# Optimization experiments

Measured on AMD Instinct MI355X. Metric: run time of the kernel, lower is better.

## Reference

```python
import jax, jax.numpy as jnp
import numpy as np

NH = 8        # num_heads
KS = 64       # key_size
C_IN = 256
C_OUT = 3 * NH * KS   # 1536
GROUPS = 3 * NH       # 24
EPS = 1e-5
H = W = 64


def setup_inputs() -> dict:
    key = jax.random.key(0)
    k1, k2 = jax.random.split(key)
    x = jax.random.normal(k1, (1, C_IN, H, W), dtype=jnp.float32)
    conv_w = jax.random.normal(k2, (C_OUT, C_IN, 1, 1), dtype=jnp.float32) * 0.05
    gn_w = jnp.ones((C_OUT,), dtype=jnp.float32)
    gn_b = jnp.zeros((C_OUT,), dtype=jnp.float32)
    return {"x": x, "conv_w": conv_w, "gn_w": gn_w, "gn_b": gn_b}


def reference(x, conv_w, gn_w, gn_b):
    B, _, h, w = x.shape
    # 1x1 conv (normalize=True -> no bias): per-pixel GEMM over channels
    attn = jnp.einsum('bchw,oc->bohw', x, conv_w[:, :, 0, 0])  # [B, 1536, H, W]
    # GroupNorm: 24 groups of KS channels, normalized over (KS, H, W)
    g = attn.reshape(B, GROUPS, -1)
    mean = g.mean(axis=-1, keepdims=True)
    var = g.var(axis=-1, keepdims=True)
    g = (g - mean) * jax.lax.rsqrt(var + EPS)
    attn = g.reshape(B, C_OUT, h, w) * gn_w[None, :, None, None] + gn_b[None, :, None, None]
    # split into key, query, value (in that order, per chunk(3, dim=2))
    attn = attn.reshape(B, NH, 3 * KS, h * w)
    key_, query, value = jnp.split(attn, 3, axis=2)   # each [B, NH, KS, HW]
    # saliency = q^T @ k / sqrt(KS) -> [B, NH, HW, HW]
    saliency = jnp.einsum('bnkq,bnkl->bnql', query, key_) / jnp.sqrt(jnp.float32(KS))
    mask = jax.nn.softmax(saliency, axis=-1)
    # out = v @ mask^T -> [B, NH, KS, HW]
    out = jnp.einsum('bnkl,bnql->bnkq', value, mask)
    return out.reshape(B, NH * KS, h, w)
```

## Files before the change

kernel.cpp:

```cpp
#include <hip/hip_runtime.h>

typedef __bf16 bf16;
typedef __bf16 bf16x8 __attribute__((ext_vector_type(8)));
typedef __bf16 bf16x4 __attribute__((ext_vector_type(4)));
typedef float f32x4 __attribute__((ext_vector_type(4)));
typedef float f32x16 __attribute__((ext_vector_type(16)));


#define QF 0.18033688011112042f
#define EXPF(x) __builtin_amdgcn_exp2f(x)
#define MFMA32(A, B, C) __builtin_amdgcn_mfma_f32_32x32x16_bf16(A, B, C, 0, 0, 0)

union U4 { bf16x4 v; unsigned u[2]; };
union U8 { bf16x8 v; unsigned u[4]; };

__global__ void k_misc(const float* __restrict__ x, const float* __restrict__ w,
                       bf16* __restrict__ xT, bf16* __restrict__ wb, float* __restrict__ cs) {
    int b = blockIdx.x;
    if (b < 256) {
        __shared__ float ld[64][65];
        int cb = (b & 3) * 64;
        int pb = (b >> 2) * 64;
        int tp = (threadIdx.x & 15) * 4;
        int tc = threadIdx.x >> 4;
#pragma unroll
        for (int pass = 0; pass < 4; pass++) {
            int c = tc + pass * 16;
            float4 f = *(const float4*)(x + (cb + c) * 4096 + pb + tp);
            ld[tp][c] = f.x; ld[tp + 1][c] = f.y; ld[tp + 2][c] = f.z; ld[tp + 3][c] = f.w;
        }
        __syncthreads();
        int px = threadIdx.x >> 3;
        int co = (threadIdx.x & 7) * 8;
#pragma unroll
        for (int pass = 0; pass < 2; pass++) {
            int p2 = px + pass * 32;
            bf16x8 o;
#pragma unroll
            for (int j = 0; j < 8; j++) o[j] = (bf16)ld[p2][co + j];
            *(bf16x8*)(xT + (pb + p2) * 256 + cb + co) = o;
        }
    } else if (b < 640) {
        int idx = ((b - 256) * 256 + threadIdx.x) * 4;
        float4 f = *(const float4*)(w + idx);
        bf16x4 o;
        o[0] = (bf16)f.x; o[1] = (bf16)f.y; o[2] = (bf16)f.z; o[3] = (bf16)f.w;
        *(bf16x4*)(wb + idx) = o;
    } else {
#pragma unroll
        for (int i = 0; i < 12; i++) cs[i * 256 + threadIdx.x] = 0.f;
    }
}

__global__ __launch_bounds__(256) void k_conv(const bf16* __restrict__ Wb,
                                              const bf16* __restrict__ xT,
                                              bf16* __restrict__ qkvT,
                                              float* __restrict__ cs) {
    __shared__ __attribute__((aligned(16))) bf16 xs[64 * 72];
    __shared__ __attribute__((aligned(16))) bf16 ws2[64 * 72];
    int wid = threadIdx.x >> 6, lane = threadIdx.x & 63;
    int quad = lane >> 4, l15 = lane & 15;
    int g  = blockIdx.x % 24;
    int pb = (blockIdx.x / 24) * 64;
    int h = g / 3, sec = g % 3;
    int ob = g * 64;

    int srow = threadIdx.x >> 2;
    int scol = (threadIdx.x & 3) * 16;

    f32x4 acc[4];
#pragma unroll
    for (int c = 0; c < 4; c++) acc[c] = (f32x4){0.f, 0.f, 0.f, 0.f};

    bf16x8 fx0 = *(const bf16x8*)(xT + (pb + srow) * 256 + scol);
    bf16x8 fx1 = *(const bf16x8*)(xT + (pb + srow) * 256 + scol + 8);
    bf16x8 fw0 = *(const bf16x8*)(Wb + (ob + srow) * 256 + scol);
    bf16x8 fw1 = *(const bf16x8*)(Wb + (ob + srow) * 256 + scol + 8);

    for (int c4 = 0; c4 < 4; c4++) {
        __syncthreads();
        *(bf16x8*)(xs  + srow * 72 + scol)     = fx0;
        *(bf16x8*)(xs  + srow * 72 + scol + 8) = fx1;
        *(bf16x8*)(ws2 + srow * 72 + scol)     = fw0;
        *(bf16x8*)(ws2 + srow * 72 + scol + 8) = fw1;
        __syncthreads();

        if (c4 < 3) {
            int co = (c4 + 1) * 64;
            fx0 = *(const bf16x8*)(xT + (pb + srow) * 256 + co + scol);
            fx1 = *(const bf16x8*)(xT + (pb + srow) * 256 + co + scol + 8);
            fw0 = *(const bf16x8*)(Wb + (ob + srow) * 256 + co + scol);
            fw1 = *(const bf16x8*)(Wb + (ob + srow) * 256 + co + scol + 8);
        }

#pragma unroll
        for (int k2 = 0; k2 < 2; k2++) {
            bf16x8 a = *(const bf16x8*)(ws2 + (wid * 16 + l15) * 72 + k2 * 32 + quad * 8);
#pragma unroll
            for (int c = 0; c < 4; c++) {
                bf16x8 b = *(const bf16x8*)(xs + (c * 16 + l15) * 72 + k2 * 32 + quad * 8);
                acc[c] = __builtin_amdgcn_mfma_f32_16x16x32_bf16(a, b, acc[c], 0, 0, 0);
            }
        }
    }

    int ch0 = wid * 16 + quad * 4;
#pragma unroll
    for (int r = 0; r < 4; r++) {
        float sp  = acc[0][r] + acc[1][r] + acc[2][r] + acc[3][r];
        float ssp = acc[0][r] * acc[0][r] + acc[1][r] * acc[1][r]
                  + acc[2][r] * acc[2][r] + acc[3][r] * acc[3][r];
#pragma unroll
        for (int m = 1; m < 16; m <<= 1) {
            sp  += __shfl_xor(sp,  m, 64);
            ssp += __shfl_xor(ssp, m, 64);
        }
        if (l15 == 0) {
            atomicAdd(cs + (ob + ch0 + r) * 2,     sp);
            atomicAdd(cs + (ob + ch0 + r) * 2 + 1, ssp);
        }
    }

    __syncthreads();
    bf16* tile = xs;
    if (sec == 2) {
#pragma unroll
        for (int c = 0; c < 4; c++)
#pragma unroll
            for (int r = 0; r < 4; r++)
                tile[(ch0 + r) * 72 + c * 16 + l15] = (bf16)acc[c][r];
    } else {
#pragma unroll
        for (int c = 0; c < 4; c++) {
            bf16x4 o;
#pragma unroll
            for (int r = 0; r < 4; r++) o[r] = (bf16)acc[c][r];
            *(bf16x4*)(&tile[(c * 16 + l15) * 72 + ch0]) = o;
        }
    }
    __syncthreads();
    bf16* base = qkvT + h * 786432;
    int t = threadIdx.x;
    if (sec == 2) {
        bf16* V = base + 524288;
#pragma unroll
        for (int it = 0; it < 2; it++) {
            int e = it * 256 + t; int ch = e >> 3; int pxo = (e & 7) * 8;
            *(bf16x8*)(V + ch * 4096 + pb + pxo) = *(const bf16x8*)(&tile[ch * 72 + pxo]);
        }
    } else {
        bf16* dst = base + (sec == 0 ? 262144 : 0);
#pragma unroll
        for (int it = 0; it < 2; it++) {
            int e = it * 256 + t; int px = e >> 3; int cho = (e & 7) * 8;
            *(bf16x8*)(dst + (pb + px) * 64 + cho) = *(const bf16x8*)(&tile[px * 72 + cho]);
        }
    }
}

#define PF_BLOCK(S, LACC, PFA, PFB)                                             \
    {                                                                           \
        float p0 = EXPF(S[0]),  p1 = EXPF(S[1]),  p2 = EXPF(S[2]),  p3 = EXPF(S[3]);   \
        float p4 = EXPF(S[4]),  p5 = EXPF(S[5]),  p6 = EXPF(S[6]),  p7 = EXPF(S[7]);   \
        float p8 = EXPF(S[8]),  p9 = EXPF(S[9]),  p10 = EXPF(S[10]), p11 = EXPF(S[11]); \
        float p12 = EXPF(S[12]), p13 = EXPF(S[13]), p14 = EXPF(S[14]), p15 = EXPF(S[15]); \
        LACC += (((p0 + p1) + (p2 + p3)) + ((p4 + p5) + (p6 + p7)))             \
              + (((p8 + p9) + (p10 + p11)) + ((p12 + p13) + (p14 + p15)));      \
        U4 lo, hi;                                                              \
        lo.v[0] = (bf16)p0;  lo.v[1] = (bf16)p1;  lo.v[2] = (bf16)p2;  lo.v[3] = (bf16)p3;  \
        hi.v[0] = (bf16)p4;  hi.v[1] = (bf16)p5;  hi.v[2] = (bf16)p6;  hi.v[3] = (bf16)p7;  \
        unsigned a0 = lo.u[0], b0 = hi.u[0], a1 = lo.u[1], b1 = hi.u[1];        \
        asm("v_permlane32_swap_b32 %0, %1" : "+v"(a0), "+v"(b0));               \
        asm("v_permlane32_swap_b32 %0, %1" : "+v"(a1), "+v"(b1));               \
        U8 fA; fA.u[0] = a0; fA.u[1] = a1; fA.u[2] = b0; fA.u[3] = b1;          \
        PFA = fA.v;                                                             \
        U4 lo2, hi2;                                                            \
        lo2.v[0] = (bf16)p8;  lo2.v[1] = (bf16)p9;  lo2.v[2] = (bf16)p10; lo2.v[3] = (bf16)p11; \
        hi2.v[0] = (bf16)p12; hi2.v[1] = (bf16)p13; hi2.v[2] = (bf16)p14; hi2.v[3] = (bf16)p15; \
        unsigned a2 = lo2.u[0], b2 = hi2.u[0], a3 = lo2.u[1], b3 = hi2.u[1];    \
        asm("v_permlane32_swap_b32 %0, %1" : "+v"(a2), "+v"(b2));               \
        asm("v_permlane32_swap_b32 %0, %1" : "+v"(a3), "+v"(b3));               \
        U8 fB; fB.u[0] = a2; fB.u[1] = a3; fB.u[2] = b2; fB.u[3] = b3;          \
        PFB = fB.v;                                                             \
    }

#define STAGE(BK, BV)                                                           \
    *(bf16x8*)((BK) + r0 * 72 + koff)        = kf0;                             \
    *(bf16x8*)((BK) + (r0 + 32) * 72 + koff) = kf1;                             \
    *(bf16x8*)((BV) + r0 * 72 + koff)        = vf0;                             \
    *(bf16x8*)((BV) + (r0 + 32) * 72 + koff) = vf1;

#define PREFETCH(T)                                                             \
    {   int nb = (T) * 64;                                                      \
        kf0 = *(const bf16x8*)(KT + (nb + r0) * 64 + koff);                     \
        kf1 = *(const bf16x8*)(KT + (nb + r0 + 32) * 64 + koff);                \
        vf0 = *(const bf16x8*)(V + r0 * 4096 + nb + koff);                      \
        vf1 = *(const bf16x8*)(V + (r0 + 32) * 4096 + nb + koff); }

#define QK64(KSB)                                                               \
    {   const bf16* kra = (KSB) + l31 * 72 + half * 8;                          \
        const bf16* krb = (KSB) + (32 + l31) * 72 + half * 8;                   \
        __builtin_amdgcn_s_setprio(1);                                          \
        { bf16x8 fa = *(const bf16x8*)(kra +  0), fb = *(const bf16x8*)(krb +  0); \
          s00 = MFMA32(fa, bqA[0], s00); s01 = MFMA32(fa, bqB[0], s01);         \
          s10 = MFMA32(fb, bqA[0], s10); s11 = MFMA32(fb, bqB[0], s11); }       \
        { bf16x8 fa = *(const bf16x8*)(kra + 16), fb = *(const bf16x8*)(krb + 16); \
          s00 = MFMA32(fa, bqA[1], s00); s01 = MFMA32(fa, bqB[1], s01);         \
          s10 = MFMA32(fb, bqA[1], s10); s11 = MFMA32(fb, bqB[1], s11); }       \
        { bf16x8 fa = *(const bf16x8*)(kra + 32), fb = *(const bf16x8*)(krb + 32); \
          s00 = MFMA32(fa, bqA[2], s00); s01 = MFMA32(fa, bqB[2], s01);         \
          s10 = MFMA32(fb, bqA[2], s10); s11 = MFMA32(fb, bqB[2], s11); }       \
        { bf16x8 fa = *(const bf16x8*)(kra + 48), fb = *(const bf16x8*)(krb + 48); \
          s00 = MFMA32(fa, bqA[3], s00); s01 = MFMA32(fa, bqB[3], s01);         \
          s10 = MFMA32(fb, bqA[3], s10); s11 = MFMA32(fb, bqB[3], s11); }       \
        __builtin_amdgcn_s_setprio(0); }

#define PV64(VSB)                                                               \
    {   const bf16* vra = (VSB) + l31 * 72 + half * 8;                          \
        const bf16* vrb = (VSB) + (32 + l31) * 72 + half * 8;                   \
        __builtin_amdgcn_s_setprio(1);                                          \
        { bf16x8 fa = *(const bf16x8*)(vra +  0), fb = *(const bf16x8*)(vrb +  0); \
          oA0 = MFMA32(fa, pa0, oA0); oB0 = MFMA32(fa, pb0, oB0);               \
          oA1 = MFMA32(fb, pa0, oA1); oB1 = MFMA32(fb, pb0, oB1); }             \
        { bf16x8 fa = *(const bf16x8*)(vra + 16), fb = *(const bf16x8*)(vrb + 16); \
          oA0 = MFMA32(fa, pa1, oA0); oB0 = MFMA32(fa, pb1, oB0);               \
          oA1 = MFMA32(fb, pa1, oA1); oB1 = MFMA32(fb, pb1, oB1); }             \
        { bf16x8 fa = *(const bf16x8*)(vra + 32), fb = *(const bf16x8*)(vrb + 32); \
          oA0 = MFMA32(fa, pa2, oA0); oB0 = MFMA32(fa, pb2, oB0);               \
          oA1 = MFMA32(fb, pa2, oA1); oB1 = MFMA32(fb, pb2, oB1); }             \
        { bf16x8 fa = *(const bf16x8*)(vra + 48), fb = *(const bf16x8*)(vrb + 48); \
          oA0 = MFMA32(fa, pa3, oA0); oB0 = MFMA32(fa, pb3, oB0);               \
          oA1 = MFMA32(fb, pa3, oA1); oB1 = MFMA32(fb, pb3, oB1); }             \
        __builtin_amdgcn_s_setprio(0); }

__global__ __launch_bounds__(256, 2) void k_attn(const bf16* __restrict__ qkvT,
                                                 const float2* __restrict__ cs,
                                                 const float* __restrict__ gnw,
                                                 const float* __restrict__ gnb,
                                                 bf16* __restrict__ Opart,
                                                 float* __restrict__ Lsum) {
    int bid   = blockIdx.x;
    int h     = bid & 7;
    int qb    = (bid >> 3) & 15;
    int split = bid >> 7;
    int wid = threadIdx.x >> 6, lane = threadIdx.x & 63;
    int l31 = lane & 31, half = lane >> 5;
    const bf16* QT = qkvT + h * 786432;
    const bf16* KT = QT + 262144;
    const bf16* V  = QT + 524288;
    int qw = qb * 256 + wid * 64;

    __shared__ __attribute__((aligned(16))) bf16 Ks[2][64 * 72];
    __shared__ __attribute__((aligned(16))) bf16 Vs[2][64 * 72];

    int r0   = threadIdx.x >> 3;
    int koff = (threadIdx.x & 7) * 8;

    float2 vK = cs[(h * 3) * 64 + lane];
    float2 vQ = cs[(h * 3 + 1) * 64 + lane];
    float sK = vK.x, qK = vK.y, sQ = vQ.x, qQ = vQ.y;
#pragma unroll
    for (int m = 1; m < 64; m <<= 1) {
        sK += __shfl_xor(sK, m, 64); qK += __shfl_xor(qK, m, 64);
        sQ += __shfl_xor(sQ, m, 64); qQ += __shfl_xor(qQ, m, 64);
    }
    const float N = 262144.0f;
    float meanK = sK / N, invK = rsqrtf(qK / N - meanK * meanK + 1e-5f);
    float meanQ = sQ / N, invQ = rsqrtf(qQ / N - meanQ * meanQ + 1e-5f);

    bf16x8 bqA[4], bqB[4];
#pragma unroll
    for (int ks = 0; ks < 4; ks++) {
        bf16x8 rawA = *(const bf16x8*)(QT + (qw + l31) * 64 + ks * 16 + half * 8);
        bf16x8 rawB = *(const bf16x8*)(QT + (qw + 32 + l31) * 64 + ks * 16 + half * 8);
#pragma unroll
        for (int j = 0; j < 8; j++) {
            int c = ks * 16 + half * 8 + j;
            float gwq = gnw[h * 192 + 64 + c] * invQ;
            float bvq = (gnb[h * 192 + 64 + c] - meanQ * gwq) * QF;
            float avq = gwq * QF;
            float aKc = gnw[h * 192 + c] * invK;
            bqA[ks][j] = (bf16)(aKc * (avq * (float)rawA[j] + bvq));
            bqB[ks][j] = (bf16)(aKc * (avq * (float)rawB[j] + bvq));
        }
    }

    f32x16 oA0 = (f32x16)(0.0f), oA1 = (f32x16)(0.0f);
    f32x16 oB0 = (f32x16)(0.0f), oB1 = (f32x16)(0.0f);
    f32x16 s00, s01, s10, s11;
    bf16x8 pa0, pa1, pa2, pa3, pb0, pb1, pb2, pb3;
    float ls0 = 0.f, ls1 = 0.f;

    int t0 = split * 16, t1 = t0 + 16;

    bf16x8 kf0, kf1, vf0, vf1;
    PREFETCH(t0);

    for (int lt = t0; lt < t1; lt++) {
        bf16* ksb = Ks[lt & 1];
        bf16* vsb = Vs[lt & 1];
        STAGE(ksb, vsb);
        __syncthreads();
        if (lt + 1 < t1) PREFETCH(lt + 1);

        s00 = (f32x16)(0.0f); s01 = (f32x16)(0.0f);
        s10 = (f32x16)(0.0f); s11 = (f32x16)(0.0f);
        QK64(ksb);

        {
            float la0 = ls0, la1 = ls1;
            PF_BLOCK(s00, la0, pa0, pa1);
            PF_BLOCK(s10, la0, pa2, pa3);
            PF_BLOCK(s01, la1, pb0, pb1);
            PF_BLOCK(s11, la1, pb2, pb3);
            ls0 = la0; ls1 = la1;
        }

        PV64(vsb);
    }

    ls0 += __shfl_xor(ls0, 32, 64);
    ls1 += __shfl_xor(ls1, 32, 64);
    if (half == 0) {
        Lsum[split * 32768 + h * 4096 + qw + l31]      = ls0;
        Lsum[split * 32768 + h * 4096 + qw + 32 + l31] = ls1;
    }

    bf16* Ob = Opart + split * 2097152;
#pragma unroll
    for (int r = 0; r < 16; r++) {
        int kd = (r & 3) + 8 * (r >> 2) + 4 * half;
        Ob[(h * 64 + kd) * 4096 + qw + l31]           = (bf16)oA0[r];
        Ob[(h * 64 + 32 + kd) * 4096 + qw + l31]      = (bf16)oA1[r];
        Ob[(h * 64 + kd) * 4096 + qw + 32 + l31]      = (bf16)oB0[r];
        Ob[(h * 64 + 32 + kd) * 4096 + qw + 32 + l31] = (bf16)oB1[r];
    }
}

__global__ void k_final(const bf16* __restrict__ Opart, const float* __restrict__ Lsum,
                        const float2* __restrict__ cs, const float* __restrict__ gnw,
                        const float* __restrict__ gnb, float* __restrict__ out) {
    int gid = blockIdx.x * 256 + threadIdx.x;
    int row = gid >> 9;
    int c8  = (gid & 511) << 3;
    int h   = row >> 6;

    int g = h * 3 + 2;
    int c = threadIdx.x & 63;
    float2 v = cs[g * 64 + c];
    float s = v.x, ss = v.y;
#pragma unroll
    for (int m = 1; m < 64; m <<= 1) { s += __shfl_xor(s, m, 64); ss += __shfl_xor(ss, m, 64); }
    const float N = 262144.0f;
    float mean = s / N;
    float inv  = rsqrtf(ss / N - mean * mean + 1e-5f);
    int gi = h * 192 + 128 + (row & 63);
    float gw = gnw[gi];
    float va = inv * gw;
    float vb = gnb[gi] - mean * inv * gw;

    float o[8] = {0, 0, 0, 0, 0, 0, 0, 0};
    float l[8] = {0, 0, 0, 0, 0, 0, 0, 0};
#pragma unroll
    for (int sp = 0; sp < 4; sp++) {
        bf16x8 vv = *(const bf16x8*)(Opart + sp * 2097152 + row * 4096 + c8);
        const float* L = Lsum + sp * 32768 + h * 4096 + c8;
        float4 l0 = *(const float4*)L;
        float4 l1 = *(const float4*)(L + 4);
#pragma unroll
        for (int j = 0; j < 8; j++) o[j] += (float)vv[j];
        l[0] += l0.x; l[1] += l0.y; l[2] += l0.z; l[3] += l0.w;
        l[4] += l1.x; l[5] += l1.y; l[6] += l1.z; l[7] += l1.w;
    }
    float4 r0, r1;
    r0.x = va * o[0] / l[0] + vb; r0.y = va * o[1] / l[1] + vb;
    r0.z = va * o[2] / l[2] + vb; r0.w = va * o[3] / l[3] + vb;
    r1.x = va * o[4] / l[4] + vb; r1.y = va * o[5] / l[5] + vb;
    r1.z = va * o[6] / l[6] + vb; r1.w = va * o[7] / l[7] + vb;
    *(float4*)(out + row * 4096 + c8)     = r0;
    *(float4*)(out + row * 4096 + c8 + 4) = r1;
}

extern "C" void kernel_launch(void* const* d_in, const int* in_sizes, int n_in,
                              void* d_out, int out_size, void* d_ws, size_t ws_size,
                              hipStream_t stream) {
    const float* x      = (const float*)d_in[0];
    const float* conv_w = (const float*)d_in[1];
    const float* gn_w   = (const float*)d_in[2];
    const float* gn_b   = (const float*)d_in[3];
    float* out = (float*)d_out;
    char* ws = (char*)d_ws;

    bf16*   qkvT  = (bf16*) (ws);
    bf16*   Opart = (bf16*) (ws + 12582912);
    bf16*   Wb    = (bf16*) (ws + 12582912);
    bf16*   xT    = (bf16*) (ws + 13369344);
    float*  Lsum  = (float*)(ws + 29360128);
    float*  cs    = (float*)(ws + 29884416);

    hipLaunchKernelGGL(k_misc,  dim3(641),  dim3(256), 0, stream, x, conv_w, xT, Wb, cs);
    hipLaunchKernelGGL(k_conv,  dim3(1536), dim3(256), 0, stream, Wb, xT, qkvT, cs);
    hipLaunchKernelGGL(k_attn,  dim3(512),  dim3(256), 0, stream, qkvT, (const float2*)cs,
                       gn_w, gn_b, Opart, Lsum);
    hipLaunchKernelGGL(k_final, dim3(1024), dim3(256), 0, stream, Opart, Lsum, (const float2*)cs, gn_w, gn_b, out);
}
```

Baseline: 130.8 us.

## Fuse fp32-to-bf16 conversion into conv and split-combine into attention kernel

The separate cast/transpose kernel goes away: the conv kernel now reads fp32 weights and input directly, converts to bf16 and transposes x into shared memory. The final combine kernel is folded into the attention kernel with an atomic counter per (head, query block), so the last of the four split blocks reduces the partial outputs and applies GroupNorm scaling. This removes two launches and the round trip through the bf16 workspace copies. In exchange it adds fp32 global reads, scalar strided LDS stores, a memset, and a serialized tail done by the last-arriving block.

```diff
diff --git a/kernel.cpp b/kernel.cpp
--- a/kernel.cpp
+++ b/kernel.cpp
@@ -14,83 +14,77 @@
 union U4 { bf16x4 v; unsigned u[2]; };
 union U8 { bf16x8 v; unsigned u[4]; };
 
-__global__ void k_misc(const float* __restrict__ x, const float* __restrict__ w,
-                       bf16* __restrict__ xT, bf16* __restrict__ wb, float* __restrict__ cs) {
-    int b = blockIdx.x;
-    if (b < 256) {
-        __shared__ float ld[64][65];
-        int cb = (b & 3) * 64;
-        int pb = (b >> 2) * 64;
-        int tp = (threadIdx.x & 15) * 4;
-        int tc = threadIdx.x >> 4;
-#pragma unroll
-        for (int pass = 0; pass < 4; pass++) {
-            int c = tc + pass * 16;
-            float4 f = *(const float4*)(x + (cb + c) * 4096 + pb + tp);
-            ld[tp][c] = f.x; ld[tp + 1][c] = f.y; ld[tp + 2][c] = f.z; ld[tp + 3][c] = f.w;
-        }
-        __syncthreads();
-        int px = threadIdx.x >> 3;
-        int co = (threadIdx.x & 7) * 8;
-#pragma unroll
-        for (int pass = 0; pass < 2; pass++) {
-            int p2 = px + pass * 32;
-            bf16x8 o;
-#pragma unroll
-            for (int j = 0; j < 8; j++) o[j] = (bf16)ld[p2][co + j];
-            *(bf16x8*)(xT + (pb + p2) * 256 + cb + co) = o;
-        }
-    } else if (b < 640) {
-        int idx = ((b - 256) * 256 + threadIdx.x) * 4;
-        float4 f = *(const float4*)(w + idx);
-        bf16x4 o;
-        o[0] = (bf16)f.x; o[1] = (bf16)f.y; o[2] = (bf16)f.z; o[3] = (bf16)f.w;
-        *(bf16x4*)(wb + idx) = o;
-    } else {
-#pragma unroll
-        for (int i = 0; i < 12; i++) cs[i * 256 + threadIdx.x] = 0.f;
-    }
-}
-
-__global__ __launch_bounds__(256) void k_conv(const bf16* __restrict__ Wb,
-                                              const bf16* __restrict__ xT,
+__global__ __launch_bounds__(256) void k_conv(const float* __restrict__ Wf,
+                                              const float* __restrict__ xf,
                                               bf16* __restrict__ qkvT,
                                               float* __restrict__ cs) {
     __shared__ __attribute__((aligned(16))) bf16 xs[64 * 72];
     __shared__ __attribute__((aligned(16))) bf16 ws2[64 * 72];
     int wid = threadIdx.x >> 6, lane = threadIdx.x & 63;
     int quad = lane >> 4, l15 = lane & 15;
-    int g  = blockIdx.x % 24;
-    int pb = (blockIdx.x / 24) * 64;
+    int pb = (blockIdx.x & 63) * 64;
+    int g  = blockIdx.x >> 6;
     int h = g / 3, sec = g % 3;
     int ob = g * 64;
 
     int srow = threadIdx.x >> 2;
     int scol = (threadIdx.x & 3) * 16;
 
+    int xch = threadIdx.x >> 4;
+    int xpx = (threadIdx.x & 15) * 4;
+
     f32x4 acc[4];
 #pragma unroll
     for (int c = 0; c < 4; c++) acc[c] = (f32x4){0.f, 0.f, 0.f, 0.f};
 
-    bf16x8 fx0 = *(const bf16x8*)(xT + (pb + srow) * 256 + scol);
-    bf16x8 fx1 = *(const bf16x8*)(xT + (pb + srow) * 256 + scol + 8);
-    bf16x8 fw0 = *(const bf16x8*)(Wb + (ob + srow) * 256 + scol);
-    bf16x8 fw1 = *(const bf16x8*)(Wb + (ob + srow) * 256 + scol + 8);
+    float4 w0 = *(const float4*)(Wf + (ob + srow) * 256 + scol);
+    float4 w1 = *(const float4*)(Wf + (ob + srow) * 256 + scol + 4);
+    float4 w2 = *(const float4*)(Wf + (ob + srow) * 256 + scol + 8);
+    float4 w3 = *(const float4*)(Wf + (ob + srow) * 256 + scol + 12);
+    float4 xv0 = *(const float4*)(xf + (xch)      * 4096 + pb + xpx);
+    float4 xv1 = *(const float4*)(xf + (xch + 16) * 4096 + pb + xpx);
+    float4 xv2 = *(const float4*)(xf + (xch + 32) * 4096 + pb + xpx);
+    float4 xv3 = *(const float4*)(xf + (xch + 48) * 4096 + pb + xpx);
 
     for (int c4 = 0; c4 < 4; c4++) {
         __syncthreads();
-        *(bf16x8*)(xs  + srow * 72 + scol)     = fx0;
-        *(bf16x8*)(xs  + srow * 72 + scol + 8) = fx1;
-        *(bf16x8*)(ws2 + srow * 72 + scol)     = fw0;
-        *(bf16x8*)(ws2 + srow * 72 + scol + 8) = fw1;
+        {
+            bf16x8 a, b;
+            a[0] = (bf16)w0.x; a[1] = (bf16)w0.y; a[2] = (bf16)w0.z; a[3] = (bf16)w0.w;
+            a[4] = (bf16)w1.x; a[5] = (bf16)w1.y; a[6] = (bf16)w1.z; a[7] = (bf16)w1.w;
+            b[0] = (bf16)w2.x; b[1] = (bf16)w2.y; b[2] = (bf16)w2.z; b[3] = (bf16)w2.w;
+            b[4] = (bf16)w3.x; b[5] = (bf16)w3.y; b[6] = (bf16)w3.z; b[7] = (bf16)w3.w;
+            *(bf16x8*)(ws2 + srow * 72 + scol)     = a;
+            *(bf16x8*)(ws2 + srow * 72 + scol + 8) = b;
+        }
+        xs[(xpx + 0) * 72 + xch]      = (bf16)xv0.x;
+        xs[(xpx + 1) * 72 + xch]      = (bf16)xv0.y;
+        xs[(xpx + 2) * 72 + xch]      = (bf16)xv0.z;
+        xs[(xpx + 3) * 72 + xch]      = (bf16)xv0.w;
+        xs[(xpx + 0) * 72 + xch + 16] = (bf16)xv1.x;
+        xs[(xpx + 1) * 72 + xch + 16] = (bf16)xv1.y;
+        xs[(xpx + 2) * 72 + xch + 16] = (bf16)xv1.z;
+        xs[(xpx + 3) * 72 + xch + 16] = (bf16)xv1.w;
+        xs[(xpx + 0) * 72 + xch + 32] = (bf16)xv2.x;
+        xs[(xpx + 1) * 72 + xch + 32] = (bf16)xv2.y;
+        xs[(xpx + 2) * 72 + xch + 32] = (bf16)xv2.z;
+        xs[(xpx + 3) * 72 + xch + 32] = (bf16)xv2.w;
+        xs[(xpx + 0) * 72 + xch + 48] = (bf16)xv3.x;
+        xs[(xpx + 1) * 72 + xch + 48] = (bf16)xv3.y;
+        xs[(xpx + 2) * 72 + xch + 48] = (bf16)xv3.z;
+        xs[(xpx + 3) * 72 + xch + 48] = (bf16)xv3.w;
         __syncthreads();
 
         if (c4 < 3) {
             int co = (c4 + 1) * 64;
-            fx0 = *(const bf16x8*)(xT + (pb + srow) * 256 + co + scol);
-            fx1 = *(const bf16x8*)(xT + (pb + srow) * 256 + co + scol + 8);
-            fw0 = *(const bf16x8*)(Wb + (ob + srow) * 256 + co + scol);
-            fw1 = *(const bf16x8*)(Wb + (ob + srow) * 256 + co + scol + 8);
+            w0 = *(const float4*)(Wf + (ob + srow) * 256 + co + scol);
+            w1 = *(const float4*)(Wf + (ob + srow) * 256 + co + scol + 4);
+            w2 = *(const float4*)(Wf + (ob + srow) * 256 + co + scol + 8);
+            w3 = *(const float4*)(Wf + (ob + srow) * 256 + co + scol + 12);
+            xv0 = *(const float4*)(xf + (co + xch)      * 4096 + pb + xpx);
+            xv1 = *(const float4*)(xf + (co + xch + 16) * 4096 + pb + xpx);
+            xv2 = *(const float4*)(xf + (co + xch + 32) * 4096 + pb + xpx);
+            xv3 = *(const float4*)(xf + (co + xch + 48) * 4096 + pb + xpx);
         }
 
 #pragma unroll
@@ -238,7 +232,9 @@
                                                  const float* __restrict__ gnw,
                                                  const float* __restrict__ gnb,
                                                  bf16* __restrict__ Opart,
-                                                 float* __restrict__ Lsum) {
+                                                 float* __restrict__ Lsum,
+                                                 int* __restrict__ cnt,
+                                                 float* __restrict__ out) {
     int bid   = blockIdx.x;
     int h     = bid & 7;
     int qb    = (bid >> 3) & 15;
@@ -252,6 +248,7 @@
 
     __shared__ __attribute__((aligned(16))) bf16 Ks[2][64 * 72];
     __shared__ __attribute__((aligned(16))) bf16 Vs[2][64 * 72];
+    __shared__ int lastFlag;
 
     int r0   = threadIdx.x >> 3;
     int koff = (threadIdx.x & 7) * 8;
@@ -335,50 +332,54 @@
         Ob[(h * 64 + kd) * 4096 + qw + 32 + l31]      = (bf16)oB0[r];
         Ob[(h * 64 + 32 + kd) * 4096 + qw + 32 + l31] = (bf16)oB1[r];
     }
-}
-
-__global__ void k_final(const bf16* __restrict__ Opart, const float* __restrict__ Lsum,
-                        const float2* __restrict__ cs, const float* __restrict__ gnw,
-                        const float* __restrict__ gnb, float* __restrict__ out) {
-    int gid = blockIdx.x * 256 + threadIdx.x;
-    int row = gid >> 9;
-    int c8  = (gid & 511) << 3;
-    int h   = row >> 6;
-
-    int g = h * 3 + 2;
-    int c = threadIdx.x & 63;
-    float2 v = cs[g * 64 + c];
-    float s = v.x, ss = v.y;
-#pragma unroll
-    for (int m = 1; m < 64; m <<= 1) { s += __shfl_xor(s, m, 64); ss += __shfl_xor(ss, m, 64); }
-    const float N = 262144.0f;
-    float mean = s / N;
-    float inv  = rsqrtf(ss / N - mean * mean + 1e-5f);
-    int gi = h * 192 + 128 + (row & 63);
-    float gw = gnw[gi];
-    float va = inv * gw;
-    float vb = gnb[gi] - mean * inv * gw;
-
-    float o[8] = {0, 0, 0, 0, 0, 0, 0, 0};
-    float l[8] = {0, 0, 0, 0, 0, 0, 0, 0};
-#pragma unroll
-    for (int sp = 0; sp < 4; sp++) {
-        bf16x8 vv = *(const bf16x8*)(Opart + sp * 2097152 + row * 4096 + c8);
-        const float* L = Lsum + sp * 32768 + h * 4096 + c8;
-        float4 l0 = *(const float4*)L;
-        float4 l1 = *(const float4*)(L + 4);
-#pragma unroll
-        for (int j = 0; j < 8; j++) o[j] += (float)vv[j];
-        l[0] += l0.x; l[1] += l0.y; l[2] += l0.z; l[3] += l0.w;
-        l[4] += l1.x; l[5] += l1.y; l[6] += l1.z; l[7] += l1.w;
-    }
-    float4 r0, r1;
-    r0.x = va * o[0] / l[0] + vb; r0.y = va * o[1] / l[1] + vb;
-    r0.z = va * o[2] / l[2] + vb; r0.w = va * o[3] / l[3] + vb;
-    r1.x = va * o[4] / l[4] + vb; r1.y = va * o[5] / l[5] + vb;
-    r1.z = va * o[6] / l[6] + vb; r1.w = va * o[7] / l[7] + vb;
-    *(float4*)(out + row * 4096 + c8)     = r0;
-    *(float4*)(out + row * 4096 + c8 + 4) = r1;
+
+    __syncthreads();
+    if (threadIdx.x == 0) {
+        __threadfence();
+        lastFlag = atomicAdd(cnt + (h * 16 + qb), 1);
+    }
+    __syncthreads();
+    if (lastFlag == 3) {
+        __threadfence();
+        float2 vV = cs[(h * 3 + 2) * 64 + lane];
+        float sV = vV.x, qV = vV.y;
+#pragma unroll
+        for (int m = 1; m < 64; m <<= 1) {
+            sV += __shfl_xor(sV, m, 64); qV += __shfl_xor(qV, m, 64);
+        }
+        float meanV = sV / N, invV = rsqrtf(qV / N - meanV * meanV + 1e-5f);
+        int qc0 = qb * 256;
+#pragma unroll
+        for (int it = 0; it < 8; it++) {
+            int item = it * 256 + threadIdx.x;
+            int kd   = item >> 5;
+            int c8   = qc0 + (item & 31) * 8;
+            int rowg = h * 64 + kd;
+            float gw = gnw[h * 192 + 128 + kd];
+            float va = invV * gw;
+            float vb = gnb[h * 192 + 128 + kd] - meanV * invV * gw;
+            float o[8] = {0, 0, 0, 0, 0, 0, 0, 0};
+            float l[8] = {0, 0, 0, 0, 0, 0, 0, 0};
+#pragma unroll
+            for (int sp = 0; sp < 4; sp++) {
+                bf16x8 vv = *(const bf16x8*)(Opart + sp * 2097152 + rowg * 4096 + c8);
+                const float* L = Lsum + sp * 32768 + h * 4096 + c8;
+                float4 l0 = *(const float4*)L;
+                float4 l1 = *(const float4*)(L + 4);
+#pragma unroll
+                for (int j = 0; j < 8; j++) o[j] += (float)vv[j];
+                l[0] += l0.x; l[1] += l0.y; l[2] += l0.z; l[3] += l0.w;
+                l[4] += l1.x; l[5] += l1.y; l[6] += l1.z; l[7] += l1.w;
+            }
+            float4 r0o, r1o;
+            r0o.x = va * o[0] / l[0] + vb; r0o.y = va * o[1] / l[1] + vb;
+            r0o.z = va * o[2] / l[2] + vb; r0o.w = va * o[3] / l[3] + vb;
+            r1o.x = va * o[4] / l[4] + vb; r1o.y = va * o[5] / l[5] + vb;
+            r1o.z = va * o[6] / l[6] + vb; r1o.w = va * o[7] / l[7] + vb;
+            *(float4*)(out + rowg * 4096 + c8)     = r0o;
+            *(float4*)(out + rowg * 4096 + c8 + 4) = r1o;
+        }
+    }
 }
 
 extern "C" void kernel_launch(void* const* d_in, const int* in_sizes, int n_in,
@@ -393,14 +394,12 @@
 
     bf16*   qkvT  = (bf16*) (ws);
     bf16*   Opart = (bf16*) (ws + 12582912);
-    bf16*   Wb    = (bf16*) (ws + 12582912);
-    bf16*   xT    = (bf16*) (ws + 13369344);
     float*  Lsum  = (float*)(ws + 29360128);
     float*  cs    = (float*)(ws + 29884416);
-
-    hipLaunchKernelGGL(k_misc,  dim3(641),  dim3(256), 0, stream, x, conv_w, xT, Wb, cs);
-    hipLaunchKernelGGL(k_conv,  dim3(1536), dim3(256), 0, stream, Wb, xT, qkvT, cs);
-    hipLaunchKernelGGL(k_attn,  dim3(512),  dim3(256), 0, stream, qkvT, (const float2*)cs,
-                       gn_w, gn_b, Opart, Lsum);
-    hipLaunchKernelGGL(k_final, dim3(1024), dim3(256), 0, stream, Opart, Lsum, (const float2*)cs, gn_w, gn_b, out);
+    int*    cnt   = (int*)  (ws + 29896704);
+
+    hipMemsetAsync(ws + 29884416, 0, 12800, stream);
+    hipLaunchKernelGGL(k_conv, dim3(1536), dim3(256), 0, stream, conv_w, x, qkvT, cs);
+    hipLaunchKernelGGL(k_attn, dim3(512),  dim3(256), 0, stream, qkvT, (const float2*)cs,
+                       gn_w, gn_b, Opart, Lsum, cnt, out);
 }
```

Result: slower. 182.7 us (+39.7%).

## Software-pipeline attention loop: overlap next QK with previous tile's PV

Applied to the files above, without the earlier changes.

Restructures the attention inner loop so each iteration issues the QK MFMAs for tile t, then the PV MFMAs for tile t-1, then the softmax for tile t. Independent matrix work can then hide the latency of the exp/convert softmax section. A prologue and epilogue handle the first QK and last PV. A second __syncthreads per iteration is added so the double-buffered V tile is not overwritten while still in use. This costs an extra barrier and keeps more accumulators and P fragments live, which raises register pressure under launch_bounds(256,2).

```diff
diff --git a/kernel.cpp b/kernel.cpp
--- a/kernel.cpp
+++ b/kernel.cpp
@@ -200,6 +200,8 @@
 #define QK64(KSB)                                                               \
     {   const bf16* kra = (KSB) + l31 * 72 + half * 8;                          \
         const bf16* krb = (KSB) + (32 + l31) * 72 + half * 8;                   \
+        s00 = (f32x16)(0.0f); s01 = (f32x16)(0.0f);                             \
+        s10 = (f32x16)(0.0f); s11 = (f32x16)(0.0f);                             \
         __builtin_amdgcn_s_setprio(1);                                          \
         { bf16x8 fa = *(const bf16x8*)(kra +  0), fb = *(const bf16x8*)(krb +  0); \
           s00 = MFMA32(fa, bqA[0], s00); s01 = MFMA32(fa, bqB[0], s01);         \
@@ -233,6 +235,14 @@
           oA1 = MFMA32(fb, pa3, oA1); oB1 = MFMA32(fb, pb3, oB1); }             \
         __builtin_amdgcn_s_setprio(0); }
 
+#define SOFTMAX_ALL()                                                           \
+    {   float la0 = ls0, la1 = ls1;                                             \
+        PF_BLOCK(s00, la0, pa0, pa1);                                           \
+        PF_BLOCK(s10, la0, pa2, pa3);                                           \
+        PF_BLOCK(s01, la1, pb0, pb1);                                           \
+        PF_BLOCK(s11, la1, pb2, pb3);                                           \
+        ls0 = la0; ls1 = la1; }
+
 __global__ __launch_bounds__(256, 2) void k_attn(const bf16* __restrict__ qkvT,
                                                  const float2* __restrict__ cs,
                                                  const float* __restrict__ gnw,
@@ -296,28 +306,22 @@
     bf16x8 kf0, kf1, vf0, vf1;
     PREFETCH(t0);
 
-    for (int lt = t0; lt < t1; lt++) {
-        bf16* ksb = Ks[lt & 1];
-        bf16* vsb = Vs[lt & 1];
-        STAGE(ksb, vsb);
+    STAGE(Ks[t0 & 1], Vs[t0 & 1]);
+    __syncthreads();
+    PREFETCH(t0 + 1);
+    QK64(Ks[t0 & 1]);
+    SOFTMAX_ALL();
+
+    for (int lt = t0 + 1; lt < t1; lt++) {
+        __syncthreads();
+        STAGE(Ks[lt & 1], Vs[lt & 1]);
         __syncthreads();
         if (lt + 1 < t1) PREFETCH(lt + 1);
-
-        s00 = (f32x16)(0.0f); s01 = (f32x16)(0.0f);
-        s10 = (f32x16)(0.0f); s11 = (f32x16)(0.0f);
-        QK64(ksb);
-
-        {
-            float la0 = ls0, la1 = ls1;
-            PF_BLOCK(s00, la0, pa0, pa1);
-            PF_BLOCK(s10, la0, pa2, pa3);
-            PF_BLOCK(s01, la1, pb0, pb1);
-            PF_BLOCK(s11, la1, pb2, pb3);
-            ls0 = la0; ls1 = la1;
-        }
-
-        PV64(vsb);
-    }
+        QK64(Ks[lt & 1]);
+        PV64(Vs[(lt - 1) & 1]);
+        SOFTMAX_ALL();
+    }
+    PV64(Vs[(t1 - 1) & 1]);
 
     ls0 += __shfl_xor(ls0, 32, 64);
     ls1 += __shfl_xor(ls1, 32, 64);
```

Measured after the change: 130.1 us. Within noise of the previous version (-0.5%).
